# Performance work log

Measured on AMD Instinct MI355X. Metric: run time of the kernel, lower is better.

## Reference

```python
import jax, jax.numpy as jnp
import numpy as np

SIZE = 512
HEADS = 4
DK = SIZE // HEADS
CHUNK = 16
SHIFT = 8
EPS = 1e-12


def layer_norm(x, g, b):
    m = jnp.mean(x, axis=-1, keepdims=True)
    v = jnp.var(x, axis=-1, keepdims=True)
    return (x - m) / jnp.sqrt(v + EPS) * g + b


def setup_inputs() -> dict:
    key = jax.random.key(0)
    ks = jax.random.split(key, 8)
    B, L, C = 16, 2048, SIZE
    p = lambda k, shp: jax.random.normal(k, shp, jnp.float32) * 0.02
    return {
        "x": jax.random.normal(ks[0], (B, L, C), jnp.float32),
        "mask": jnp.ones((B, 1, L), jnp.float32),
        "pos_emb": jnp.zeros((1, L, C), jnp.float32),
        "mask_pad": jnp.ones((B, 1, L), jnp.float32),
        "Wq": p(ks[1], (C, C)), "bq": jnp.zeros((C,), jnp.float32),
        "Wk": p(ks[2], (C, C)), "bk": jnp.zeros((C,), jnp.float32),
        "Wv": p(ks[3], (C, C)), "bv": jnp.zeros((C,), jnp.float32),
        "Wo": p(ks[4], (C, C)), "bo": jnp.zeros((C,), jnp.float32),
        "g1": jnp.ones((C,), jnp.float32), "be1": jnp.zeros((C,), jnp.float32),
        "g2": jnp.ones((C,), jnp.float32), "be2": jnp.zeros((C,), jnp.float32),
        "W1": p(ks[5], (C, 4 * C)), "bf1": jnp.zeros((4 * C,), jnp.float32),
        "W2": p(ks[6], (4 * C, C)), "bf2": jnp.zeros((C,), jnp.float32),
    }


def reference(x, mask, pos_emb, mask_pad, Wq, bq, Wk, bk, Wv, bv, Wo, bo,
              g1, be1, g2, be2, W1, bf1, W2, bf2):
    B, L, C = x.shape
    nW = L // CHUNK
    half = CHUNK // 2
    # shifted-window attention mask, built exactly as in the torch code
    # (zeros base, -100 in the cross-shift blocks); shape (nW, CHUNK, CHUNK)
    am = jnp.zeros((nW, CHUNK, CHUNK), x.dtype)
    am = am.at[:-1, :half - 1, half:].set(-100.0)
    am = am.at[-1, half:, half:].set(-100.0)

    residual = x
    xn = layer_norm(x, g1, be1)  # normalize_before

    # cyclic shift
    sx = jnp.roll(xn, -SHIFT, axis=1)                    # (B, L, C)
    sm = jnp.roll(mask_pad[:, 0, :], -SHIFT, axis=1)     # (B, L)

    # chunk partition
    xc = sx.reshape(B, nW, CHUNK, C)
    mc = sm.reshape(B, nW, CHUNK)

    # windowed multi-head attention
    q = (xc @ Wq + bq).reshape(B, nW, CHUNK, HEADS, DK)
    k = (xc @ Wk + bk).reshape(B, nW, CHUNK, HEADS, DK)
    v = (xc @ Wv + bv).reshape(B, nW, CHUNK, HEADS, DK)
    scores = jnp.einsum('bwqhd,bwkhd->bwhqk', q, k) / jnp.sqrt(jnp.asarray(DK, x.dtype))
    scores = scores + am[None, :, None]                  # add shift mask per chunk
    valid = mc[:, :, None, None, :] > 0.0                # key padding mask
    scores = jnp.where(valid, scores, jnp.asarray(-1e30, x.dtype))
    attn = jax.nn.softmax(scores, axis=-1)
    attn = jnp.where(valid, attn, jnp.asarray(0.0, x.dtype))
    out = jnp.einsum('bwhqk,bwkhd->bwqhd', attn, v).reshape(B, nW, CHUNK, C)
    out = out @ Wo + bo

    # chunk reverse + reverse shift
    sx_out = out.reshape(B, L, C)
    xa = jnp.roll(sx_out, SHIFT, axis=1)
    m = jnp.roll(sm, SHIFT, axis=1)
    xa = xa * m[:, :, None]
    x1 = residual + xa  # dropout_rate = 0

    # feed forward block (pre-norm, ReLU FFN)
    residual2 = x1
    xn2 = layer_norm(x1, g2, be2)
    h = jax.nn.relu(xn2 @ W1 + bf1)
    x2 = residual2 + (h @ W2 + bf2)
    return x2
```

## Files before the change

### kernel.cpp

```cpp
#include <hip/hip_runtime.h>
#include <stdint.h>


typedef unsigned short bfu;

using bf16x8 = __attribute__((ext_vector_type(8))) __bf16;
using f32x4  = __attribute__((ext_vector_type(4))) float;

union U8 { uint4 v; unsigned short s[8]; };
union F4 { float4 v; float f[4]; };
union ABFrag { uint4 u; bf16x8 f; };

__device__ __forceinline__ float bf2f(unsigned short u) {
    union { uint32_t i; float f; } c; c.i = ((uint32_t)u) << 16; return c.f;
}
__device__ __forceinline__ unsigned short f2bf(float f) {
    union { float f; uint32_t i; } c; c.f = f;
    uint32_t x = c.i;
    return (unsigned short)((x + 0x7FFFu + ((x >> 16) & 1u)) >> 16);
}
__device__ __forceinline__ uint4 pack8(float4 a, float4 b) {
    U8 o;
    o.s[0] = f2bf(a.x); o.s[1] = f2bf(a.y); o.s[2] = f2bf(a.z); o.s[3] = f2bf(a.w);
    o.s[4] = f2bf(b.x); o.s[5] = f2bf(b.y); o.s[6] = f2bf(b.z); o.s[7] = f2bf(b.w);
    return o.v;
}

#define GLDS16(gp, lp)                                                        \
    __builtin_amdgcn_global_load_lds(                                         \
        (__attribute__((address_space(1))) void*)(gp),                        \
        (__attribute__((address_space(3))) void*)(lp), 16, 0, 0)


__global__ __launch_bounds__(256) void wconv_kernel(
    const float* __restrict__ W, bfu* __restrict__ Wt, int K, int N)
{
    __shared__ float t[32][33];
    const int bn = blockIdx.x << 5;
    const int bk = blockIdx.y << 5;
    const int tx = threadIdx.x & 31, ty = threadIdx.x >> 5;
#pragma unroll
    for (int i = 0; i < 32; i += 8)
        t[ty + i][tx] = W[(size_t)(bk + ty + i) * N + bn + tx];
    __syncthreads();
#pragma unroll
    for (int i = 0; i < 32; i += 8)
        Wt[(size_t)(bn + ty + i) * K + bk + tx] = f2bf(t[tx][ty + i]);
}

__global__ __launch_bounds__(256) void wconv3_kernel(
    const float* __restrict__ Wq, const float* __restrict__ Wk,
    const float* __restrict__ Wv, bfu* __restrict__ Wt)
{
    __shared__ float t[32][33];
    const int z = blockIdx.z;
    const float* W = (z == 0) ? Wq : (z == 1) ? Wk : Wv;
    bfu* Wo = Wt + (size_t)z * 512 * 512;
    const int bn = blockIdx.x << 5;
    const int bk = blockIdx.y << 5;
    const int tx = threadIdx.x & 31, ty = threadIdx.x >> 5;
#pragma unroll
    for (int i = 0; i < 32; i += 8)
        t[ty + i][tx] = W[(size_t)(bk + ty + i) * 512 + bn + tx];
    __syncthreads();
#pragma unroll
    for (int i = 0; i < 32; i += 8)
        Wo[(size_t)(bn + ty + i) * 512 + bk + tx] = f2bf(t[tx][ty + i]);
}

__global__ __launch_bounds__(256) void bias_concat_kernel(
    const float* __restrict__ a, const float* __restrict__ b,
    const float* __restrict__ c, float* __restrict__ o)
{
    const int t = blockIdx.x * 256 + threadIdx.x;
    const float* src = (t < 512) ? a : (t < 1024) ? b : c;
    o[t] = src[t & 511];
}


__global__ __launch_bounds__(256) void ln1_shift_kernel(
    const float* __restrict__ x, const float* __restrict__ g,
    const float* __restrict__ be, bfu* __restrict__ out)
{
    const int ms = (blockIdx.x << 2) + (threadIdx.x >> 6);
    const int b = ms >> 11;
    const int ls = ms & 2047;
    const int l = (ls + 8) & 2047;
    const int c0 = (threadIdx.x & 63) << 3;
    const float* xp = x + ((((size_t)(b << 11)) + l) << 9) + c0;
    F4 f0, f1; f0.v = *(const float4*)xp; f1.v = *(const float4*)(xp + 4);
    float vv[8]; float s = 0.f, sq = 0.f;
#pragma unroll
    for (int j = 0; j < 4; ++j) { vv[j] = f0.f[j]; vv[4 + j] = f1.f[j]; }
#pragma unroll
    for (int j = 0; j < 8; ++j) { s += vv[j]; sq += vv[j] * vv[j]; }
#pragma unroll
    for (int o = 32; o > 0; o >>= 1) { s += __shfl_xor(s, o); sq += __shfl_xor(sq, o); }
    const float mean = s * (1.f / 512.f);
    float var = sq * (1.f / 512.f) - mean * mean;
    var = fmaxf(var, 0.f);
    const float rstd = rsqrtf(var + 1e-12f);
    F4 g0, g1v, b0, b1;
    g0.v = *(const float4*)(g + c0);  g1v.v = *(const float4*)(g + c0 + 4);
    b0.v = *(const float4*)(be + c0); b1.v = *(const float4*)(be + c0 + 4);
    U8 o8;
#pragma unroll
    for (int j = 0; j < 4; ++j) {
        o8.s[j]     = f2bf((vv[j]     - mean) * rstd * g0.f[j]  + b0.f[j]);
        o8.s[4 + j] = f2bf((vv[4 + j] - mean) * rstd * g1v.f[j] + b1.f[j]);
    }
    *(uint4*)(out + (((size_t)ms) << 9) + c0) = o8.v;
}

__global__ __launch_bounds__(256) void ln2_kernel(
    const bfu* __restrict__ x1, const float* __restrict__ g,
    const float* __restrict__ be, bfu* __restrict__ out)
{
    const int ms = (blockIdx.x << 2) + (threadIdx.x >> 6);
    const int c0 = (threadIdx.x & 63) << 3;
    U8 u; u.v = *(const uint4*)(x1 + (((size_t)ms) << 9) + c0);
    float vv[8]; float s = 0.f, sq = 0.f;
#pragma unroll
    for (int j = 0; j < 8; ++j) { float f = bf2f(u.s[j]); vv[j] = f; s += f; sq += f * f; }
#pragma unroll
    for (int o = 32; o > 0; o >>= 1) { s += __shfl_xor(s, o); sq += __shfl_xor(sq, o); }
    const float mean = s * (1.f / 512.f);
    float var = sq * (1.f / 512.f) - mean * mean;
    var = fmaxf(var, 0.f);
    const float rstd = rsqrtf(var + 1e-12f);
    F4 g0, g1v, b0, b1;
    g0.v = *(const float4*)(g + c0);  g1v.v = *(const float4*)(g + c0 + 4);
    b0.v = *(const float4*)(be + c0); b1.v = *(const float4*)(be + c0 + 4);
    U8 o8;
#pragma unroll
    for (int j = 0; j < 4; ++j) {
        o8.s[j]     = f2bf((vv[j]     - mean) * rstd * g0.f[j]  + b0.f[j]);
        o8.s[4 + j] = f2bf((vv[4 + j] - mean) * rstd * g1v.f[j] + b1.f[j]);
    }
    *(uint4*)(out + (((size_t)ms) << 9) + c0) = o8.v;
}


template<int EPI>
__global__ __launch_bounds__(512, 2) void mgemm(
    const bfu* __restrict__ X, const bfu* __restrict__ Wt,
    const float* __restrict__ bias,
    bfu* Ob, float* Ofl,
    const float* __restrict__ xres, const bfu* __restrict__ prevb,
    const float* __restrict__ maskpad,
    int M, int N, int K)
{
    __shared__ __align__(16) char smem[131072];
    bfu* smb = (bfu*)smem;
    const char* smc = (const char*)smem;
    float* epi = (float*)smem;

    const int t = threadIdx.x;
    const int lane = t & 63;
    const int w = t >> 6;
    const int wm = w >> 2, wn = w & 3;
    const int q = lane >> 4, l15 = lane & 15;

    const int gx = gridDim.x;
    const int nwg = gx * gridDim.y;
    int wid = blockIdx.y * gx + blockIdx.x;
    wid = ((wid & 7) * (nwg >> 3)) + (wid >> 3);
    const int row0 = (wid / gx) << 8;
    const int col0 = (wid % gx) << 8;

    const int srow = (w << 3) + (lane >> 3);
    const int scol = (((lane & 7) ^ ((lane >> 3) & 7)) << 3);
    const bfu* gA = X  + (size_t)(row0 + srow) * K + scol;
    const bfu* gB = Wt + (size_t)(col0 + srow) * K + scol;
    bfu* lsA0 = smb + (w << 9) + (lane << 3);
    bfu* lsB0 = lsA0 + 16384;
    bfu* lsA1 = lsA0 + 32768;
    bfu* lsB1 = lsA0 + 49152;

    const int arow = ((wm << 7) + l15) << 7;
    const int brow = ((wn << 6) + l15) << 7;
    const int qb   = q << 4;
    const int swz  = (l15 & 7) << 4;

    f32x4 acc[8][4];
    float bv[4];
#pragma unroll
    for (int j = 0; j < 4; ++j) bv[j] = bias[col0 + (wn << 6) + (j << 4) + l15];
#pragma unroll
    for (int i = 0; i < 8; ++i)
#pragma unroll
        for (int j = 0; j < 4; ++j) {
            acc[i][j][0] = bv[j]; acc[i][j][1] = bv[j];
            acc[i][j][2] = bv[j]; acc[i][j][3] = bv[j];
        }

    ABFrag a[4][2];
    ABFrag bb[2][2][2];

#define SB_   __builtin_amdgcn_s_barrier()
#define VM8_  asm volatile("s_waitcnt vmcnt(8)" ::: "memory")
#define VM0_  asm volatile("s_waitcnt vmcnt(0)" ::: "memory")
#define VMNOP_ do {} while (0)

#define LDA_(D, MH)                                                           \
    _Pragma("unroll") for (int mf = 0; mf < 4; ++mf)                          \
    _Pragma("unroll") for (int kk = 0; kk < 2; ++kk)                          \
        a[mf][kk].u = *(const uint4*)(smc + (D)*65536 + arow + (MH)*8192 +    \
                                      mf*2048 + (((kk << 6) + qb) ^ swz));
#define LDB_(D, NH)                                                           \
    _Pragma("unroll") for (int nf = 0; nf < 2; ++nf)                          \
    _Pragma("unroll") for (int kk = 0; kk < 2; ++kk)                          \
        bb[NH][nf][kk].u = *(const uint4*)(smc + (D)*65536 + 32768 + brow +   \
                                      (NH)*4096 + nf*2048 +                   \
                                      (((kk << 6) + qb) ^ swz));
#define MFMAQ_(MH, NH)                                                        \
    __builtin_amdgcn_s_setprio(1);                                            \
    _Pragma("unroll") for (int mf = 0; mf < 4; ++mf)                          \
    _Pragma("unroll") for (int nf = 0; nf < 2; ++nf) {                        \
        acc[(MH)*4+mf][(NH)*2+nf] = __builtin_amdgcn_mfma_f32_16x16x32_bf16(  \
            a[mf][0].f, bb[NH][nf][0].f, acc[(MH)*4+mf][(NH)*2+nf], 0, 0, 0); \
        acc[(MH)*4+mf][(NH)*2+nf] = __builtin_amdgcn_mfma_f32_16x16x32_bf16(  \
            a[mf][1].f, bb[NH][nf][1].f, acc[(MH)*4+mf][(NH)*2+nf], 0, 0, 0);}\
    __builtin_amdgcn_s_setprio(0);
#define STGA4_(D, GA2) do {                                                   \
    GLDS16((GA2), lsA##D);                                                    \
    GLDS16((GA2) + (size_t)64  * K, lsA##D + 4096);                           \
    GLDS16((GA2) + (size_t)128 * K, lsA##D + 8192);                           \
    GLDS16((GA2) + (size_t)192 * K, lsA##D + 12288); } while (0)
#define STGB4_(D, GB2) do {                                                   \
    GLDS16((GB2), lsB##D);                                                    \
    GLDS16((GB2) + (size_t)64  * K, lsB##D + 4096);                           \
    GLDS16((GB2) + (size_t)128 * K, lsB##D + 8192);                           \
    GLDS16((GB2) + (size_t)192 * K, lsB##D + 12288); } while (0)
#define TILE_(D, DOSTG, VMW) do {                                             \
    SB_;                                                                      \
    LDA_(D, 0); LDB_(D, 0);                                                   \
    MFMAQ_(0, 0);                                                             \
    SB_;                                                                      \
    LDB_(D, 1);                                                               \
    MFMAQ_(0, 1);                                                             \
    SB_;                                                                      \
    LDA_(D, 1);                                                               \
    if (DOSTG) STGB4_(D, gB2);                                                \
    MFMAQ_(1, 0);                                                             \
    SB_;                                                                      \
    if (DOSTG) STGA4_(D, gA2);                                                \
    MFMAQ_(1, 1);                                                             \
    VMW;                                                                      \
} while (0)

    const int nT = K >> 6;

    STGA4_(0, gA); STGB4_(0, gB);
    {
        const bfu* ga1 = gA + 64; const bfu* gb1 = gB + 64;
        STGA4_(1, ga1); STGB4_(1, gb1);
    }
    VM8_;

    const bfu* gA2 = gA + 128;
    const bfu* gB2 = gB + 128;
#pragma unroll 1
    for (int tt = 0; tt < nT - 2; tt += 2) {
        TILE_(0, true, VM8_);
        gA2 += 64; gB2 += 64;
        TILE_(1, true, VM8_);
        gA2 += 64; gB2 += 64;
    }
    TILE_(0, false, VM0_);
    TILE_(1, false, VMNOP_);

#undef LDA_
#undef LDB_
#undef MFMAQ_
#undef STGA4_
#undef STGB4_
#undef TILE_

    SB_;

    float* epw = epi + w * 1088;
    const int c8 = (lane & 7) << 3;
    const int r8 = lane >> 3;
    const int colg = col0 + (wn << 6) + c8;
#pragma unroll
    for (int i = 0; i < 8; ++i) {
#pragma unroll
        for (int j = 0; j < 4; ++j)
#pragma unroll
            for (int r = 0; r < 4; ++r) {
                float y = acc[i][j][r];
                if (EPI == 1) y = fmaxf(y, 0.f);
                epw[((q << 2) + r) * 68 + (j << 4) + l15] = y;
            }
        __builtin_amdgcn_wave_barrier();
#pragma unroll
        for (int h = 0; h < 2; ++h) {
            const int rr = r8 + (h << 3);
            F4 f0, f1;
            f0.v = *(const float4*)&epw[rr * 68 + c8];
            f1.v = *(const float4*)&epw[rr * 68 + c8 + 4];
            const int row_out = row0 + (wm << 7) + (i << 4) + rr;
            if (EPI == 0 || EPI == 1) {
                *(uint4*)(Ob + (size_t)row_out * N + colg) = pack8(f0.v, f1.v);
            } else if (EPI == 2) {
                const int bb2 = row_out >> 11;
                const int ls = row_out & 2047;
                const int l = (ls + 8) & 2047;
                const float mp = maskpad[(bb2 << 11) + l];
                const size_t dst = ((size_t)(bb2 << 11) + l) * (size_t)N + colg;
                F4 x0, x1v;
                x0.v = *(const float4*)(xres + dst);
                x1v.v = *(const float4*)(xres + dst + 4);
                F4 o0, o1;
#pragma unroll
                for (int jj = 0; jj < 4; ++jj) {
                    o0.f[jj] = x0.f[jj]  + f0.f[jj] * mp;
                    o1.f[jj] = x1v.f[jj] + f1.f[jj] * mp;
                }
                *(uint4*)(Ob + dst) = pack8(o0.v, o1.v);
            } else {
                const size_t dst = (size_t)row_out * N + colg;
                U8 pb; pb.v = *(const uint4*)(prevb + dst);
                F4 o0, o1;
#pragma unroll
                for (int jj = 0; jj < 4; ++jj) {
                    o0.f[jj] = bf2f(pb.s[jj])     + f0.f[jj];
                    o1.f[jj] = bf2f(pb.s[4 + jj]) + f1.f[jj];
                }
                *(float4*)(Ofl + dst) = o0.v;
                *(float4*)(Ofl + dst + 4) = o1.v;
            }
        }
        __builtin_amdgcn_wave_barrier();
    }
}


__global__ __launch_bounds__(256) void attn_kernel(
    const bfu* __restrict__ qkv, const float* __restrict__ mpad,
    bfu* __restrict__ out)
{
    __shared__ float qs[16][132];
    __shared__ float ks[16][132];
    __shared__ float vs[16][132];
    __shared__ float ps[16][17];
    const int t = threadIdx.x;
    const int wg = blockIdx.x;
    const int h = blockIdx.y;
    const int b = wg >> 7;
    const int w = wg & 127;
    const int li = t >> 4;
    const int d0 = (t & 15) << 3;
    const size_t bi = (((size_t)wg << 4) + li) * 1536 + (h << 7) + d0;
    U8 uq, uk, uv;
    uq.v = *(const uint4*)(qkv + bi);
    uk.v = *(const uint4*)(qkv + bi + 512);
    uv.v = *(const uint4*)(qkv + bi + 1024);
    F4 a0, a1;
#pragma unroll
    for (int j = 0; j < 4; ++j) { a0.f[j] = bf2f(uq.s[j]); a1.f[j] = bf2f(uq.s[4 + j]); }
    *(float4*)&qs[li][d0] = a0.v;  *(float4*)&qs[li][d0 + 4] = a1.v;
#pragma unroll
    for (int j = 0; j < 4; ++j) { a0.f[j] = bf2f(uk.s[j]); a1.f[j] = bf2f(uk.s[4 + j]); }
    *(float4*)&ks[li][d0] = a0.v;  *(float4*)&ks[li][d0 + 4] = a1.v;
#pragma unroll
    for (int j = 0; j < 4; ++j) { a0.f[j] = bf2f(uv.s[j]); a1.f[j] = bf2f(uv.s[4 + j]); }
    *(float4*)&vs[li][d0] = a0.v;  *(float4*)&vs[li][d0 + 4] = a1.v;
    __syncthreads();
    const int qi = li, ki = t & 15;
    float s = 0.f;
#pragma unroll
    for (int d = 0; d < 128; d += 4) {
        F4 qv, kv;
        qv.v = *(const float4*)&qs[qi][d];
        kv.v = *(const float4*)&ks[ki][d];
        s += qv.f[0] * kv.f[0] + qv.f[1] * kv.f[1]
           + qv.f[2] * kv.f[2] + qv.f[3] * kv.f[3];
    }
    s *= 0.088388347648318447f;
    const bool lastw = (w == 127);
    if (lastw ? (qi >= 8 && ki >= 8) : (qi < 7 && ki >= 8)) s -= 100.f;
    const int lkey = ((w << 4) + ki + 8) & 2047;
    const bool valid = mpad[(b << 11) + lkey] > 0.f;
    if (!valid) s = -1e30f;
    float mx = s;
#pragma unroll
    for (int o = 8; o > 0; o >>= 1) mx = fmaxf(mx, __shfl_xor(mx, o, 16));
    float e = __expf(s - mx);
    float sum = e;
#pragma unroll
    for (int o = 8; o > 0; o >>= 1) sum += __shfl_xor(sum, o, 16);
    float p = e / sum;
    if (!valid) p = 0.f;
    ps[qi][ki] = p;
    __syncthreads();
    F4 o0, o1;
#pragma unroll
    for (int j = 0; j < 4; ++j) { o0.f[j] = 0.f; o1.f[j] = 0.f; }
#pragma unroll
    for (int kk = 0; kk < 16; ++kk) {
        const float pw = ps[li][kk];
        F4 v0, v1;
        v0.v = *(const float4*)&vs[kk][d0];
        v1.v = *(const float4*)&vs[kk][d0 + 4];
#pragma unroll
        for (int j = 0; j < 4; ++j) {
            o0.f[j] += pw * v0.f[j];
            o1.f[j] += pw * v1.f[j];
        }
    }
    U8 o8;
#pragma unroll
    for (int j = 0; j < 4; ++j) { o8.s[j] = f2bf(o0.f[j]); o8.s[4 + j] = f2bf(o1.f[j]); }
    *(uint4*)(out + (((size_t)wg << 4) + li) * 512 + (h << 7) + d0) = o8.v;
}


extern "C" void kernel_launch(void* const* d_in, const int* in_sizes, int n_in,
                              void* d_out, int out_size, void* d_ws, size_t ws_size,
                              hipStream_t stream)
{
    const float* x    = (const float*)d_in[0];
    const float* mpad = (const float*)d_in[3];
    const float* Wq = (const float*)d_in[4];  const float* bq = (const float*)d_in[5];
    const float* Wk = (const float*)d_in[6];  const float* bk = (const float*)d_in[7];
    const float* Wv = (const float*)d_in[8];  const float* bv = (const float*)d_in[9];
    const float* Wo = (const float*)d_in[10]; const float* bo = (const float*)d_in[11];
    const float* g1 = (const float*)d_in[12]; const float* be1 = (const float*)d_in[13];
    const float* g2 = (const float*)d_in[14]; const float* be2 = (const float*)d_in[15];
    const float* W1 = (const float*)d_in[16]; const float* bf1 = (const float*)d_in[17];
    const float* W2 = (const float*)d_in[18]; const float* bf2 = (const float*)d_in[19];
    float* out = (float*)d_out;

    char* p = (char*)d_ws;
    const size_t MB = (size_t)1 << 20;
    bfu* xn_s = (bfu*)p;
    bfu* att  = xn_s;
    bfu* qkv  = (bfu*)(p + 32 * MB);
    bfu* x1   = qkv;
    bfu* W1t  = (bfu*)(p + 64 * MB);
    bfu* W2t  = (bfu*)(p + 66 * MB);
    bfu* xn2  = (bfu*)(p + 96 * MB);
    bfu* hreg = (bfu*)(p + 128 * MB);
    bfu* Wqkvt = hreg;
    bfu* Wot   = hreg + 1536 * 512;
    float* bqkv = (float*)(hreg + 2048 * 512);

    const int M = 32768;
    dim3 blk(256);
    dim3 blk5(512);

    wconv3_kernel<<<dim3(16, 16, 3), blk, 0, stream>>>(Wq, Wk, Wv, Wqkvt);
    wconv_kernel<<<dim3(16, 16), blk, 0, stream>>>(Wo, Wot, 512, 512);
    bias_concat_kernel<<<dim3(6), blk, 0, stream>>>(bq, bk, bv, bqkv);

    ln1_shift_kernel<<<8192, blk, 0, stream>>>(x, g1, be1, xn_s);

    mgemm<0><<<dim3(6, 128), blk5, 0, stream>>>(xn_s, Wqkvt, bqkv, qkv, nullptr, nullptr, nullptr, nullptr, M, 1536, 512);

    attn_kernel<<<dim3(2048, 4), blk, 0, stream>>>(qkv, mpad, att);

    wconv_kernel<<<dim3(64, 16), blk, 0, stream>>>(W1, W1t, 512, 2048);
    wconv_kernel<<<dim3(16, 64), blk, 0, stream>>>(W2, W2t, 2048, 512);

    mgemm<2><<<dim3(2, 128), blk5, 0, stream>>>(att, Wot, bo, x1, nullptr, x, nullptr, mpad, M, 512, 512);

    ln2_kernel<<<8192, blk, 0, stream>>>(x1, g2, be2, xn2);

    mgemm<1><<<dim3(8, 128), blk5, 0, stream>>>(xn2, W1t, bf1, hreg, nullptr, nullptr, nullptr, nullptr, M, 2048, 512);
    mgemm<3><<<dim3(2, 128), blk5, 0, stream>>>(hreg, W2t, bf2, nullptr, out, nullptr, x1, nullptr, M, 512, 2048);
}
```

Measured before the change: 487.2 us.

## Shrink GEMM tiles to 128x256 with K=32 stages for higher occupancy

Reworks the shared MFMA GEMM kernel from 256x256 tiles with K-step 64 to 128x256 tiles with K-step 32. Shared memory drops from 128KB to 48KB and the accumulators are halved, so launch bounds move to 4 blocks per CU, and the grids are doubled in M. The staging layout, swizzle and load schedule are rewritten to match. The aim is more concurrent waves and better latency hiding, at the cost of less operand reuse per tile, more barriers per FLOP and extra global traffic for the weight operand.

```diff
diff --git a/kernel.cpp b/kernel.cpp
--- a/kernel.cpp
+++ b/kernel.cpp
@@ -142,7 +142,7 @@
 
 
 template<int EPI>
-__global__ __launch_bounds__(512, 2) void mgemm(
+__global__ __launch_bounds__(512, 4) void mgemm(
     const bfu* __restrict__ X, const bfu* __restrict__ Wt,
     const float* __restrict__ bias,
     bfu* Ob, float* Ofl,
@@ -150,8 +150,7 @@
     const float* __restrict__ maskpad,
     int M, int N, int K)
 {
-    __shared__ __align__(16) char smem[131072];
-    bfu* smb = (bfu*)smem;
+    __shared__ __align__(16) char smem[49152];
     const char* smc = (const char*)smem;
     float* epi = (float*)smem;
 
@@ -165,116 +164,90 @@
     const int nwg = gx * gridDim.y;
     int wid = blockIdx.y * gx + blockIdx.x;
     wid = ((wid & 7) * (nwg >> 3)) + (wid >> 3);
-    const int row0 = (wid / gx) << 8;
+    const int row0 = (wid / gx) << 7;
     const int col0 = (wid % gx) << 8;
 
-    const int srow = (w << 3) + (lane >> 3);
-    const int scol = (((lane & 7) ^ ((lane >> 3) & 7)) << 3);
-    const bfu* gA = X  + (size_t)(row0 + srow) * K + scol;
-    const bfu* gB = Wt + (size_t)(col0 + srow) * K + scol;
-    bfu* lsA0 = smb + (w << 9) + (lane << 3);
-    bfu* lsB0 = lsA0 + 16384;
-    bfu* lsA1 = lsA0 + 32768;
-    bfu* lsB1 = lsA0 + 49152;
-
-    const int arow = ((wm << 7) + l15) << 7;
-    const int brow = ((wn << 6) + l15) << 7;
-    const int qb   = q << 4;
-    const int swz  = (l15 & 7) << 4;
-
-    f32x4 acc[8][4];
+    const int srow = t >> 2;
+    const int schunk = (((lane & 3) ^ ((lane >> 3) & 3)) << 3);
+    const bfu* gAp  = X  + (size_t)(row0 + srow) * K + schunk;
+    const bfu* gB0p = Wt + (size_t)(col0 + srow) * K + schunk;
+    const bfu* gB1p = Wt + (size_t)(col0 + 128 + srow) * K + schunk;
+    bfu* lsA0  = (bfu*)smem + (t << 3);
+    bfu* lsB0  = lsA0 + 4096;
+    bfu* lsB0b = lsA0 + 8192;
+    bfu* lsA1  = lsA0 + 12288;
+    bfu* lsB1  = lsA0 + 16384;
+    bfu* lsB1b = lsA0 + 20480;
+
+    const int fswz = (q ^ ((l15 >> 1) & 3)) << 4;
+    const int abase = (((wm << 6) + l15) << 6) + fswz;
+    const int bbase = 8192 + (((wn << 6) + l15) << 6) + fswz;
+
+    f32x4 acc[4][4];
     float bv[4];
 #pragma unroll
     for (int j = 0; j < 4; ++j) bv[j] = bias[col0 + (wn << 6) + (j << 4) + l15];
 #pragma unroll
-    for (int i = 0; i < 8; ++i)
+    for (int i = 0; i < 4; ++i)
 #pragma unroll
         for (int j = 0; j < 4; ++j) {
             acc[i][j][0] = bv[j]; acc[i][j][1] = bv[j];
             acc[i][j][2] = bv[j]; acc[i][j][3] = bv[j];
         }
 
-    ABFrag a[4][2];
-    ABFrag bb[2][2][2];
+    ABFrag a[4], b[4];
 
 #define SB_   __builtin_amdgcn_s_barrier()
-#define VM8_  asm volatile("s_waitcnt vmcnt(8)" ::: "memory")
+#define VM3_  asm volatile("s_waitcnt vmcnt(3)" ::: "memory")
 #define VM0_  asm volatile("s_waitcnt vmcnt(0)" ::: "memory")
 #define VMNOP_ do {} while (0)
 
-#define LDA_(D, MH)                                                           \
+#define LDA_(D)                                                               \
     _Pragma("unroll") for (int mf = 0; mf < 4; ++mf)                          \
-    _Pragma("unroll") for (int kk = 0; kk < 2; ++kk)                          \
-        a[mf][kk].u = *(const uint4*)(smc + (D)*65536 + arow + (MH)*8192 +    \
-                                      mf*2048 + (((kk << 6) + qb) ^ swz));
-#define LDB_(D, NH)                                                           \
-    _Pragma("unroll") for (int nf = 0; nf < 2; ++nf)                          \
-    _Pragma("unroll") for (int kk = 0; kk < 2; ++kk)                          \
-        bb[NH][nf][kk].u = *(const uint4*)(smc + (D)*65536 + 32768 + brow +   \
-                                      (NH)*4096 + nf*2048 +                   \
-                                      (((kk << 6) + qb) ^ swz));
-#define MFMAQ_(MH, NH)                                                        \
+        a[mf].u = *(const uint4*)(smc + (D)*24576 + abase + mf*1024);
+#define LDB_(D)                                                               \
+    _Pragma("unroll") for (int nf = 0; nf < 4; ++nf)                          \
+        b[nf].u = *(const uint4*)(smc + (D)*24576 + bbase + nf*1024);
+#define MFMAH_(H)                                                             \
     __builtin_amdgcn_s_setprio(1);                                            \
     _Pragma("unroll") for (int mf = 0; mf < 4; ++mf)                          \
-    _Pragma("unroll") for (int nf = 0; nf < 2; ++nf) {                        \
-        acc[(MH)*4+mf][(NH)*2+nf] = __builtin_amdgcn_mfma_f32_16x16x32_bf16(  \
-            a[mf][0].f, bb[NH][nf][0].f, acc[(MH)*4+mf][(NH)*2+nf], 0, 0, 0); \
-        acc[(MH)*4+mf][(NH)*2+nf] = __builtin_amdgcn_mfma_f32_16x16x32_bf16(  \
-            a[mf][1].f, bb[NH][nf][1].f, acc[(MH)*4+mf][(NH)*2+nf], 0, 0, 0);}\
+    _Pragma("unroll") for (int nf = 2*(H); nf < 2*(H)+2; ++nf)                \
+        acc[mf][nf] = __builtin_amdgcn_mfma_f32_16x16x32_bf16(                \
+            a[mf].f, b[nf].f, acc[mf][nf], 0, 0, 0);                          \
     __builtin_amdgcn_s_setprio(0);
-#define STGA4_(D, GA2) do {                                                   \
-    GLDS16((GA2), lsA##D);                                                    \
-    GLDS16((GA2) + (size_t)64  * K, lsA##D + 4096);                           \
-    GLDS16((GA2) + (size_t)128 * K, lsA##D + 8192);                           \
-    GLDS16((GA2) + (size_t)192 * K, lsA##D + 12288); } while (0)
-#define STGB4_(D, GB2) do {                                                   \
-    GLDS16((GB2), lsB##D);                                                    \
-    GLDS16((GB2) + (size_t)64  * K, lsB##D + 4096);                           \
-    GLDS16((GB2) + (size_t)128 * K, lsB##D + 8192);                           \
-    GLDS16((GB2) + (size_t)192 * K, lsB##D + 12288); } while (0)
+#define STG3_(D) do {                                                         \
+    GLDS16(gAp,  lsA##D);                                                     \
+    GLDS16(gB0p, lsB##D);                                                     \
+    GLDS16(gB1p, lsB##D##b);                                                  \
+    gAp += 32; gB0p += 32; gB1p += 32; } while (0)
 #define TILE_(D, DOSTG, VMW) do {                                             \
     SB_;                                                                      \
-    LDA_(D, 0); LDB_(D, 0);                                                   \
-    MFMAQ_(0, 0);                                                             \
+    LDA_(D); LDB_(D);                                                         \
+    MFMAH_(0);                                                                \
     SB_;                                                                      \
-    LDB_(D, 1);                                                               \
-    MFMAQ_(0, 1);                                                             \
-    SB_;                                                                      \
-    LDA_(D, 1);                                                               \
-    if (DOSTG) STGB4_(D, gB2);                                                \
-    MFMAQ_(1, 0);                                                             \
-    SB_;                                                                      \
-    if (DOSTG) STGA4_(D, gA2);                                                \
-    MFMAQ_(1, 1);                                                             \
+    if (DOSTG) STG3_(D);                                                      \
+    MFMAH_(1);                                                                \
     VMW;                                                                      \
 } while (0)
 
-    const int nT = K >> 6;
-
-    STGA4_(0, gA); STGB4_(0, gB);
-    {
-        const bfu* ga1 = gA + 64; const bfu* gb1 = gB + 64;
-        STGA4_(1, ga1); STGB4_(1, gb1);
-    }
-    VM8_;
-
-    const bfu* gA2 = gA + 128;
-    const bfu* gB2 = gB + 128;
+    const int nT = K >> 5;
+
+    STG3_(0);
+    STG3_(1);
+    VM3_;
+
 #pragma unroll 1
     for (int tt = 0; tt < nT - 2; tt += 2) {
-        TILE_(0, true, VM8_);
-        gA2 += 64; gB2 += 64;
-        TILE_(1, true, VM8_);
-        gA2 += 64; gB2 += 64;
+        TILE_(0, true, VM3_);
+        TILE_(1, true, VM3_);
     }
     TILE_(0, false, VM0_);
     TILE_(1, false, VMNOP_);
 
 #undef LDA_
 #undef LDB_
-#undef MFMAQ_
-#undef STGA4_
-#undef STGB4_
+#undef MFMAH_
+#undef STG3_
 #undef TILE_
 
     SB_;
@@ -284,7 +257,7 @@
     const int r8 = lane >> 3;
     const int colg = col0 + (wn << 6) + c8;
 #pragma unroll
-    for (int i = 0; i < 8; ++i) {
+    for (int i = 0; i < 4; ++i) {
 #pragma unroll
         for (int j = 0; j < 4; ++j)
 #pragma unroll
@@ -300,7 +273,7 @@
             F4 f0, f1;
             f0.v = *(const float4*)&epw[rr * 68 + c8];
             f1.v = *(const float4*)&epw[rr * 68 + c8 + 4];
-            const int row_out = row0 + (wm << 7) + (i << 4) + rr;
+            const int row_out = row0 + (wm << 6) + (i << 4) + rr;
             if (EPI == 0 || EPI == 1) {
                 *(uint4*)(Ob + (size_t)row_out * N + colg) = pack8(f0.v, f1.v);
             } else if (EPI == 2) {
@@ -457,17 +430,17 @@
 
     ln1_shift_kernel<<<8192, blk, 0, stream>>>(x, g1, be1, xn_s);
 
-    mgemm<0><<<dim3(6, 128), blk5, 0, stream>>>(xn_s, Wqkvt, bqkv, qkv, nullptr, nullptr, nullptr, nullptr, M, 1536, 512);
+    mgemm<0><<<dim3(6, 256), blk5, 0, stream>>>(xn_s, Wqkvt, bqkv, qkv, nullptr, nullptr, nullptr, nullptr, M, 1536, 512);
 
     attn_kernel<<<dim3(2048, 4), blk, 0, stream>>>(qkv, mpad, att);
 
     wconv_kernel<<<dim3(64, 16), blk, 0, stream>>>(W1, W1t, 512, 2048);
     wconv_kernel<<<dim3(16, 64), blk, 0, stream>>>(W2, W2t, 2048, 512);
 
-    mgemm<2><<<dim3(2, 128), blk5, 0, stream>>>(att, Wot, bo, x1, nullptr, x, nullptr, mpad, M, 512, 512);
+    mgemm<2><<<dim3(2, 256), blk5, 0, stream>>>(att, Wot, bo, x1, nullptr, x, nullptr, mpad, M, 512, 512);
 
     ln2_kernel<<<8192, blk, 0, stream>>>(x1, g2, be2, xn2);
 
-    mgemm<1><<<dim3(8, 128), blk5, 0, stream>>>(xn2, W1t, bf1, hreg, nullptr, nullptr, nullptr, nullptr, M, 2048, 512);
-    mgemm<3><<<dim3(2, 128), blk5, 0, stream>>>(hreg, W2t, bf2, nullptr, out, nullptr, x1, nullptr, M, 512, 2048);
-}
+    mgemm<1><<<dim3(8, 256), blk5, 0, stream>>>(xn2, W1t, bf1, hreg, nullptr, nullptr, nullptr, nullptr, M, 2048, 512);
+    mgemm<3><<<dim3(2, 256), blk5, 0, stream>>>(hreg, W2t, bf2, nullptr, out, nullptr, x1, nullptr, M, 512, 2048);
+}
```

New measurement: 505.6 us. 1.04x slower.
